# Kernel tuning notes

Measured on AMD Instinct MI355X. Metric: run time of the kernel, lower is better.

Reference implementation:

```python
import jax, jax.numpy as jnp
import numpy as np

LN_EPS = 1e-5


def _forward(x, conv_w, conv_b, ln_w, ln_b, in_proj_w, in_proj_b, out_proj_w, out_proj_b):
    # x: (1, duration, dimensions)
    B, Dur, Dim = x.shape
    xt = jnp.transpose(x, (0, 2, 1))  # (1, Dim, Dur) -> Conv1d NCH layout
    branches = []
    for b in range(Dur):  # structural loop over the 32 conv branches (kernel size k=b+1)
        k = b + 1
        L = Dur - b  # output length duration - k + 1
        w = conv_w[b, :, :, :k]  # (Dim_out, Dim_in, k); padded taps beyond k unused
        y = jax.lax.conv_general_dilated(
            xt, w, window_strides=(1,), padding='VALID',
            dimension_numbers=('NCH', 'OIH', 'NCH'))  # (1, Dim, L)
        y = y + conv_b[b][None, :, None]
        y = jax.nn.gelu(y, approximate=False)  # torch nn.GELU default is exact erf form
        # LayerNorm(normalized_shape=[1, Dim, L]) with batch==1 normalizes the whole tensor
        mu = jnp.mean(y)
        var = jnp.var(y)  # biased, matching torch LayerNorm
        y = (y - mu) * jax.lax.rsqrt(var + LN_EPS)
        y = y * ln_w[b, :, :L][None] + ln_b[b, :, :L][None]
        branches.append(y)  # dropout is identity at inference (p=0.0)
    xc = jnp.concatenate(branches, axis=2)  # (1, Dim, T), T = Dur*(Dur+1)//2
    T = xc.shape[2]

    # nn.MultiheadAttention(embed_dim=T, num_heads=T), batch_first=False: input (L=1, N=Dim, E=T).
    # With seq_len==1, softmax over the single key is exactly 1, so attention output is
    # out_proj(v_proj(value)). value_i = x[:, i, :] broadcast over N, so every batch row of
    # output_i equals out_proj(v_proj(xc[0, i])). Summing over i (the feature loop):
    Wv = in_proj_w[2 * T:]          # (T, T) value slice of in_proj
    bv = in_proj_b[2 * T:]          # (T,)
    V = xc[0] @ Wv.T + bv           # (Dim, T): row i is v-proj of feature i
    S = V.sum(axis=0) @ out_proj_w.T + Dim * out_proj_b  # (T,)  sum over the Dim-term loop
    xa = jnp.broadcast_to(S[None, None, :], (1, Dim, T))  # identical rows, as in torch

    # x.unfold(2, Dur, 4*Dur).mean(-1)
    step = 4 * Dur
    n_w = (T - Dur) // step + 1
    idx = jnp.arange(n_w)[:, None] * step + jnp.arange(Dur)[None, :]  # (n_w, Dur)
    pooled = xa[:, :, idx].mean(-1)  # (1, Dim, n_w)
    return jnp.transpose(pooled, (0, 2, 1))  # (1, n_w, Dim)


def setup_inputs() -> dict:
    key = jax.random.key(0)
    ks = jax.random.split(key, 6)
    Dur, Dim = 32, 256
    T = Dur * (Dur + 1) // 2  # 528
    x = jax.random.normal(ks[0], (1, Dur, Dim), jnp.float32)
    conv_w = jax.random.normal(ks[1], (Dur, Dim, Dim, Dur), jnp.float32) * 0.02  # padded kernel bank
    conv_b = jax.random.normal(ks[2], (Dur, Dim), jnp.float32) * 0.02
    ln_w = jnp.ones((Dur, Dim, Dur), jnp.float32)   # branch b uses [:, :, :Dur-b]
    ln_b = jnp.zeros((Dur, Dim, Dur), jnp.float32)
    in_proj_w = jax.random.normal(ks[3], (3 * T, T), jnp.float32) * 0.02
    in_proj_b = jnp.zeros((3 * T,), jnp.float32)
    out_proj_w = jax.random.normal(ks[4], (T, T), jnp.float32) * 0.02
    out_proj_b = jnp.zeros((T,), jnp.float32)
    return {"x": x, "conv_w": conv_w, "conv_b": conv_b, "ln_w": ln_w, "ln_b": ln_b,
            "in_proj_w": in_proj_w, "in_proj_b": in_proj_b,
            "out_proj_w": out_proj_w, "out_proj_b": out_proj_b}


def reference(x, conv_w, conv_b, ln_w, ln_b, in_proj_w, in_proj_b, out_proj_w, out_proj_b):
    return _forward(x, conv_w, conv_b, ln_w, ln_b, in_proj_w, in_proj_b, out_proj_w, out_proj_b)
```

## Files before the change

kernel.cpp:

```cpp
#include <hip/hip_runtime.h>
#include <math.h>

#define DUR 32
#define DIM 256
#define TT  528

#define WS_BSUM 0
#define WS_BSQ  32
#define WS_CY   64
#define WS_CW   592
#define WS_CB   1120
#define WS_S    1648
#define WS_ZERO_FLOATS 1648

__device__ __forceinline__ float gelu_exact(float v) {
    return 0.5f * v * (1.0f + erff(v * 0.70710678118654752f));
}

__global__ __launch_bounds__(256) void conv_kernel(
    const float* __restrict__ x, const float* __restrict__ W,
    const float* __restrict__ convb, const float* __restrict__ lnw,
    const float* __restrict__ lnb, float* ws)
{
    const int n  = threadIdx.x;
    const int bb = blockIdx.x >> 8;
    const int o  = blockIdx.x & 255;
    const int k  = bb + 1;
    const int L  = 32 - bb;

    float xv[36];
#pragma unroll
    for (int tau = 0; tau < 32; ++tau) xv[tau] = x[tau * DIM + n];
    xv[32] = 0.f; xv[33] = 0.f; xv[34] = 0.f; xv[35] = 0.f;

    const float* wrow = W + ((size_t)(bb * DIM + o) * DIM + n) * (size_t)DUR;
    float wv[32];
    const int k4 = (k + 3) >> 2;
#pragma unroll
    for (int m = 0; m < 8; ++m) {
        if (m < k4) {
            const float4 v = *(const float4*)(wrow + 4 * m);
            wv[4*m+0] = v.x; wv[4*m+1] = v.y; wv[4*m+2] = v.z; wv[4*m+3] = v.w;
        } else {
            wv[4*m+0] = 0.f; wv[4*m+1] = 0.f; wv[4*m+2] = 0.f; wv[4*m+3] = 0.f;
        }
    }
#pragma unroll
    for (int j = 0; j < 32; ++j) { if (j >= k) wv[j] = 0.f; }

    float acc[32];
#pragma unroll
    for (int t = 0; t < 32; ++t) acc[t] = 0.f;

#pragma unroll
    for (int t = 0; t < 32; ++t) {
        if (t < L) {
#pragma unroll
            for (int m = 0; m < 8; ++m) {
                if (4 * m < k) {
                    acc[t] = fmaf(xv[t + 4*m + 0], wv[4*m + 0], acc[t]);
                    acc[t] = fmaf(xv[t + 4*m + 1], wv[4*m + 1], acc[t]);
                    acc[t] = fmaf(xv[t + 4*m + 2], wv[4*m + 2], acc[t]);
                    acc[t] = fmaf(xv[t + 4*m + 3], wv[4*m + 3], acc[t]);
                }
            }
        }
    }

    const int wave = n >> 6;
    const int lane = n & 63;
    __shared__ float red[128];

#pragma unroll
    for (int t = 0; t < 32; ++t) {
        if (t < L) {
            float v = acc[t];
            v += __shfl_down(v, 32, 64);
            v += __shfl_down(v, 16, 64);
            v += __shfl_down(v, 8, 64);
            v += __shfl_down(v, 4, 64);
            v += __shfl_down(v, 2, 64);
            v += __shfl_down(v, 1, 64);
            acc[t] = v;
        }
    }
    if (lane == 0) {
#pragma unroll
        for (int t = 0; t < 32; ++t) { if (t < L) red[wave * 32 + t] = acc[t]; }
    }
    __syncthreads();

    if (n < 64) {
        float g = 0.f;
        if (n < L) {
            const float y = red[n] + red[32 + n] + red[64 + n] + red[96 + n]
                          + convb[bb * DIM + o];
            g = gelu_exact(y);
            const float lw = lnw[(size_t)(bb * DIM + o) * DUR + n];
            const float lb = lnb[(size_t)(bb * DIM + o) * DUR + n];
            const int tg = bb * 32 - (bb * (bb - 1)) / 2 + n;
            atomicAdd(ws + WS_CY + tg, g * lw);
            atomicAdd(ws + WS_CW + tg, lw);
            atomicAdd(ws + WS_CB + tg, lb);
        }
        float s1 = g, s2 = g * g;
        s1 += __shfl_down(s1, 32, 64); s2 += __shfl_down(s2, 32, 64);
        s1 += __shfl_down(s1, 16, 64); s2 += __shfl_down(s2, 16, 64);
        s1 += __shfl_down(s1, 8, 64);  s2 += __shfl_down(s2, 8, 64);
        s1 += __shfl_down(s1, 4, 64);  s2 += __shfl_down(s2, 4, 64);
        s1 += __shfl_down(s1, 2, 64);  s2 += __shfl_down(s2, 2, 64);
        s1 += __shfl_down(s1, 1, 64);  s2 += __shfl_down(s2, 1, 64);
        if (n == 0) {
            atomicAdd(ws + WS_BSUM + bb, s1);
            atomicAdd(ws + WS_BSQ + bb, s2);
        }
    }
}

__global__ __launch_bounds__(256) void proj1_kernel(
    float* ws, const float* __restrict__ in_proj_w,
    const float* __restrict__ in_proj_b)
{
    __shared__ float cc[TT];
    __shared__ float mu_s[32], r_s[32];
    __shared__ int map[TT];
    const int n = threadIdx.x;
    if (n < 32) {
        const int Lb = 32 - n;
        const float cnt = 256.f * (float)Lb;
        const float mu = ws[WS_BSUM + n] / cnt;
        const float var = ws[WS_BSQ + n] / cnt - mu * mu;
        mu_s[n] = mu;
        r_s[n] = rsqrtf(var + 1e-5f);
        const int off = n * 32 - (n * (n - 1)) / 2;
        for (int t = 0; t < Lb; ++t) map[off + t] = n;
    }
    __syncthreads();
    for (int t = n; t < TT; t += 256) {
        const int b = map[t];
        cc[t] = (ws[WS_CY + t] - mu_s[b] * ws[WS_CW + t]) * r_s[b] + ws[WS_CB + t];
    }
    __syncthreads();
    const int wave = n >> 6, lane = n & 63;
    const int row = blockIdx.x * 4 + wave;
    const float* Wr = in_proj_w + (size_t)(2 * TT + row) * TT;
    float a = 0.f;
    for (int t = lane; t < TT; t += 64) a = fmaf(Wr[t], cc[t], a);
    a += __shfl_down(a, 32, 64);
    a += __shfl_down(a, 16, 64);
    a += __shfl_down(a, 8, 64);
    a += __shfl_down(a, 4, 64);
    a += __shfl_down(a, 2, 64);
    a += __shfl_down(a, 1, 64);
    if (lane == 0) ws[WS_S + row] = a + 256.f * in_proj_b[2 * TT + row];
}

__global__ __launch_bounds__(256) void proj2_kernel(
    const float* __restrict__ ws, const float* __restrict__ out_proj_w,
    const float* __restrict__ out_proj_b, float* __restrict__ out)
{
    __shared__ float sv[TT];
    __shared__ float Sacc[32];
    __shared__ float meanv;
    const int n = threadIdx.x;
    for (int t = n; t < TT; t += 256) sv[t] = ws[WS_S + t];
    __syncthreads();
    const int wave = n >> 6, lane = n & 63;
#pragma unroll
    for (int jj = 0; jj < 8; ++jj) {
        const int j = wave * 8 + jj;
        const int u = blockIdx.x * 128 + j;
        const float* Or = out_proj_w + (size_t)u * TT;
        float a = 0.f;
        for (int t = lane; t < TT; t += 64) a = fmaf(Or[t], sv[t], a);
        a += __shfl_down(a, 32, 64);
        a += __shfl_down(a, 16, 64);
        a += __shfl_down(a, 8, 64);
        a += __shfl_down(a, 4, 64);
        a += __shfl_down(a, 2, 64);
        a += __shfl_down(a, 1, 64);
        if (lane == 0) Sacc[j] = a + 256.f * out_proj_b[u];
    }
    __syncthreads();
    if (n == 0) {
        float m = 0.f;
        for (int j = 0; j < 32; ++j) m += Sacc[j];
        meanv = m * (1.0f / 32.0f);
    }
    __syncthreads();
    out[blockIdx.x * 256 + n] = meanv;
}

extern "C" void kernel_launch(void* const* d_in, const int* in_sizes, int n_in,
                              void* d_out, int out_size, void* d_ws, size_t ws_size,
                              hipStream_t stream)
{
    const float* x   = (const float*)d_in[0];
    const float* W   = (const float*)d_in[1];
    const float* cb  = (const float*)d_in[2];
    const float* lnw = (const float*)d_in[3];
    const float* lnb = (const float*)d_in[4];
    const float* ipw = (const float*)d_in[5];
    const float* ipb = (const float*)d_in[6];
    const float* opw = (const float*)d_in[7];
    const float* opb = (const float*)d_in[8];
    float* ws  = (float*)d_ws;
    float* out = (float*)d_out;

    hipMemsetAsync(ws, 0, WS_ZERO_FLOATS * sizeof(float), stream);
    conv_kernel<<<32 * 256, 256, 0, stream>>>(x, W, cb, lnw, lnb, ws);
    proj1_kernel<<<132, 256, 0, stream>>>(ws, ipw, ipb);
    proj2_kernel<<<4, 256, 0, stream>>>(ws, opw, opb, out);
}
```

Before: 492.0 us.

## Process four output channels per conv block with double-buffered weight loads

Each conv block now computes four output channels instead of one. The x vector is loaded once per block and reused across those channels, and the weight rows for the next channel are prefetched into a second register buffer while the current one is computed. Block index ordering is also interleaved so that neighbouring blocks cover different branch sizes, which balances the uneven per-branch work. This cuts the block count by four and cuts redundant x loads. In exchange, register pressure rises and each block runs longer, which may lower occupancy.

```diff
diff --git a/kernel.cpp b/kernel.cpp
--- a/kernel.cpp
+++ b/kernel.cpp
@@ -23,82 +23,99 @@
     const float* __restrict__ lnb, float* ws)
 {
     const int n  = threadIdx.x;
-    const int bb = blockIdx.x >> 8;
-    const int o  = blockIdx.x & 255;
+    const int bb = blockIdx.x & 31;
+    const int og = blockIdx.x >> 5;
+    const int o0 = og * 4;
     const int k  = bb + 1;
     const int L  = 32 - bb;
-
-    float xv[36];
+    const int k4 = (k + 3) >> 2;
+
+    float xv[35];
 #pragma unroll
     for (int tau = 0; tau < 32; ++tau) xv[tau] = x[tau * DIM + n];
-    xv[32] = 0.f; xv[33] = 0.f; xv[34] = 0.f; xv[35] = 0.f;
-
-    const float* wrow = W + ((size_t)(bb * DIM + o) * DIM + n) * (size_t)DUR;
-    float wv[32];
-    const int k4 = (k + 3) >> 2;
-#pragma unroll
-    for (int m = 0; m < 8; ++m) {
-        if (m < k4) {
-            const float4 v = *(const float4*)(wrow + 4 * m);
-            wv[4*m+0] = v.x; wv[4*m+1] = v.y; wv[4*m+2] = v.z; wv[4*m+3] = v.w;
-        } else {
-            wv[4*m+0] = 0.f; wv[4*m+1] = 0.f; wv[4*m+2] = 0.f; wv[4*m+3] = 0.f;
-        }
-    }
-#pragma unroll
-    for (int j = 0; j < 32; ++j) { if (j >= k) wv[j] = 0.f; }
-
-    float acc[32];
-#pragma unroll
-    for (int t = 0; t < 32; ++t) acc[t] = 0.f;
-
-#pragma unroll
-    for (int t = 0; t < 32; ++t) {
-        if (t < L) {
-#pragma unroll
-            for (int m = 0; m < 8; ++m) {
-                if (4 * m < k) {
-                    acc[t] = fmaf(xv[t + 4*m + 0], wv[4*m + 0], acc[t]);
-                    acc[t] = fmaf(xv[t + 4*m + 1], wv[4*m + 1], acc[t]);
-                    acc[t] = fmaf(xv[t + 4*m + 2], wv[4*m + 2], acc[t]);
-                    acc[t] = fmaf(xv[t + 4*m + 3], wv[4*m + 3], acc[t]);
-                }
-            }
-        }
-    }
+    xv[32] = 0.f; xv[33] = 0.f; xv[34] = 0.f;
+
+    float4 wq[2][8];
+
+    auto load_w = [&](int oo, int buf) {
+        const float* wrow = W + (((size_t)(bb * DIM) + (size_t)(o0 + oo)) * DIM + n) * (size_t)DUR;
+#pragma unroll
+        for (int m = 0; m < 8; ++m) {
+            if (m < k4) {
+                wq[buf][m] = *(const float4*)(wrow + 4 * m);
+            } else {
+                wq[buf][m] = make_float4(0.f, 0.f, 0.f, 0.f);
+            }
+        }
+        {
+            float* wf = (float*)&wq[buf][0];
+#pragma unroll
+            for (int r = 0; r < 3; ++r) {
+                const int j = 4 * (k4 - 1) + 1 + r;
+                if (j >= k && j < 32) wf[j] = 0.f;
+            }
+        }
+    };
 
     const int wave = n >> 6;
     const int lane = n & 63;
-    __shared__ float red[128];
-
-#pragma unroll
-    for (int t = 0; t < 32; ++t) {
-        if (t < L) {
-            float v = acc[t];
-            v += __shfl_down(v, 32, 64);
-            v += __shfl_down(v, 16, 64);
-            v += __shfl_down(v, 8, 64);
-            v += __shfl_down(v, 4, 64);
-            v += __shfl_down(v, 2, 64);
-            v += __shfl_down(v, 1, 64);
-            acc[t] = v;
-        }
-    }
-    if (lane == 0) {
-#pragma unroll
-        for (int t = 0; t < 32; ++t) { if (t < L) red[wave * 32 + t] = acc[t]; }
-    }
-    __syncthreads();
-
-    if (n < 64) {
+    __shared__ float red[4][4][32];
+
+    load_w(0, 0);
+
+#pragma unroll
+    for (int oo = 0; oo < 4; ++oo) {
+        const int buf = oo & 1;
+        if (oo < 3) load_w(oo + 1, buf ^ 1);
+
+        float acc[32];
+#pragma unroll
+        for (int t = 0; t < 32; ++t) acc[t] = 0.f;
+
+        const float* wf = (const float*)&wq[buf][0];
+#pragma unroll
+        for (int t = 0; t < 32; ++t) {
+            if (t < L) {
+#pragma unroll
+                for (int m = 0; m < 8; ++m) {
+                    if (m < k4) {
+                        acc[t] = fmaf(xv[t + 4*m + 0], wf[4*m + 0], acc[t]);
+                        acc[t] = fmaf(xv[t + 4*m + 1], wf[4*m + 1], acc[t]);
+                        acc[t] = fmaf(xv[t + 4*m + 2], wf[4*m + 2], acc[t]);
+                        acc[t] = fmaf(xv[t + 4*m + 3], wf[4*m + 3], acc[t]);
+                    }
+                }
+            }
+        }
+
+#pragma unroll
+        for (int t = 0; t < 32; ++t) {
+            if (t < L) {
+                float v = acc[t];
+                v += __shfl_down(v, 32, 64);
+                v += __shfl_down(v, 16, 64);
+                v += __shfl_down(v, 8, 64);
+                v += __shfl_down(v, 4, 64);
+                v += __shfl_down(v, 2, 64);
+                v += __shfl_down(v, 1, 64);
+                if (lane == 0) red[oo][wave][t] = v;
+            }
+        }
+    }
+
+    __syncthreads();
+
+    {
+        const int o = o0 + wave;
         float g = 0.f;
-        if (n < L) {
-            const float y = red[n] + red[32 + n] + red[64 + n] + red[96 + n]
+        if (lane < L) {
+            const float y = red[wave][0][lane] + red[wave][1][lane]
+                          + red[wave][2][lane] + red[wave][3][lane]
                           + convb[bb * DIM + o];
             g = gelu_exact(y);
-            const float lw = lnw[(size_t)(bb * DIM + o) * DUR + n];
-            const float lb = lnb[(size_t)(bb * DIM + o) * DUR + n];
-            const int tg = bb * 32 - (bb * (bb - 1)) / 2 + n;
+            const float lw = lnw[((size_t)(bb * DIM + o)) * DUR + lane];
+            const float lb = lnb[((size_t)(bb * DIM + o)) * DUR + lane];
+            const int tg = bb * 32 - (bb * (bb - 1)) / 2 + lane;
             atomicAdd(ws + WS_CY + tg, g * lw);
             atomicAdd(ws + WS_CW + tg, lw);
             atomicAdd(ws + WS_CB + tg, lb);
@@ -110,7 +127,7 @@
         s1 += __shfl_down(s1, 4, 64);  s2 += __shfl_down(s2, 4, 64);
         s1 += __shfl_down(s1, 2, 64);  s2 += __shfl_down(s2, 2, 64);
         s1 += __shfl_down(s1, 1, 64);  s2 += __shfl_down(s2, 1, 64);
-        if (n == 0) {
+        if (lane == 0) {
             atomicAdd(ws + WS_BSUM + bb, s1);
             atomicAdd(ws + WS_BSQ + bb, s2);
         }
@@ -208,7 +225,7 @@
     float* out = (float*)d_out;
 
     hipMemsetAsync(ws, 0, WS_ZERO_FLOATS * sizeof(float), stream);
-    conv_kernel<<<32 * 256, 256, 0, stream>>>(x, W, cb, lnw, lnb, ws);
+    conv_kernel<<<32 * 64, 256, 0, stream>>>(x, W, cb, lnw, lnb, ws);
     proj1_kernel<<<132, 256, 0, stream>>>(ws, ipw, ipb);
     proj2_kernel<<<4, 256, 0, stream>>>(ws, opw, opb, out);
 }
```

New measurement: 692.2 us. 1.41x slower.
